# Performance work log

Hardware: AMD Instinct MI355X
Metric: run time of the kernel (lower is better)

The kernel has to match this reference:

```python
import jax, jax.numpy as jnp
import numpy as np


def setup_inputs() -> dict:
    key = jax.random.key(0)
    ks = jax.random.split(key, 6)
    B, H, N, C, O, G = 4, 24, 512, 120, 512, 5
    x = jax.random.normal(ks[0], (B, H, N, C), dtype=jnp.float32)
    t_indices = jnp.arange(H, dtype=jnp.int64)
    time_emb = jax.random.normal(ks[1], (H, 8), dtype=jnp.float32)
    # kaiming-uniform-ish init for base linear weight
    fan_in = C + 8
    bound = float(np.sqrt(6.0 / fan_in))
    base_w = jax.random.uniform(ks[2], (O, C + 8), minval=-bound, maxval=bound, dtype=jnp.float32)
    base_b = jax.random.uniform(ks[3], (O,), minval=-1.0 / np.sqrt(fan_in), maxval=1.0 / np.sqrt(fan_in), dtype=jnp.float32)
    spline_weight = jax.random.uniform(ks[4], (O, C + 8, G), minval=-0.1, maxval=0.1, dtype=jnp.float32)
    return {"x": x, "t_indices": t_indices, "time_emb": time_emb,
            "base_w": base_w, "base_b": base_b, "spline_weight": spline_weight}


def reference(x, t_indices, time_emb, base_w, base_b, spline_weight):
    B, H, N, C = x.shape
    G = spline_weight.shape[-1]
    grid = jnp.linspace(-1.0, 1.0, G, dtype=x.dtype)  # non-trainable buffer
    # time embedding lookup, broadcast over batch and nodes: [B,H,N,8]
    t_emb = jnp.broadcast_to(time_emb[t_indices][None, :, None, :], (B, H, N, time_emb.shape[-1]))
    x_in = jnp.concatenate([x, t_emb], axis=-1)  # [B,H,N,C+8]
    # base path: SiLU then linear
    base = jnp.einsum('bhni,oi->bhno', jax.nn.silu(x_in), base_w) + base_b
    # RBF basis: [B,H,N,C+8,G]
    inv_h = (G - 1) / 2.0  # 1 / (2/(G-1))
    basis = jnp.exp(-(((x_in[..., None] - grid) * inv_h) ** 2))
    spline = jnp.einsum('bhnig,oig->bhno', basis, spline_weight)
    return base + spline
```

## Files before the change

### kernel.cpp

```cpp
#include <hip/hip_runtime.h>
#include <hip/hip_bf16.h>

typedef __attribute__((ext_vector_type(4))) float f32x4;
typedef __attribute__((ext_vector_type(8))) short bf16x8;

#define GLDS16(gp, lp) __builtin_amdgcn_global_load_lds( \
    (__attribute__((address_space(1))) void*)(void*)(gp), \
    (__attribute__((address_space(3))) void*)(lp), 16, 0, 0)

static constexpr int Mtot = 49152;
static constexpr int Otot = 512;
static constexpr int Hh   = 24;

__device__ inline unsigned short f2bf(float f) {
    __hip_bfloat16 h = __float2bfloat16(f);
    unsigned short u;
    __builtin_memcpy(&u, &h, 2);
    return u;
}

static constexpr float C1 = 0.36787944117f;
static constexpr float C4 = 0.01831563889f;

__global__ __launch_bounds__(256) void prep_W(
        const float* __restrict__ bw, const float* __restrict__ sw,
        uint4* __restrict__ Wt)
{
    const int tid = blockIdx.x * 256 + threadIdx.x;
    const int col = tid & 511;
    const int cc  = tid >> 9;
    const int k0  = cc * 8;
    const float scale[6] = {1.0f, C4, C1, 1.0f, C1, C4};
    unsigned short s[8];
    #pragma unroll
    for (int e = 0; e < 8; ++e) {
        const int k = k0 + e;
        const int i = k / 6, f = k - i * 6;
        const float v = (f == 0) ? bw[col * 128 + i]
                                 : sw[(col * 128 + i) * 5 + (f - 1)] * scale[f];
        s[e] = f2bf(v);
    }
    uint4 u;
    u.x = s[0] | ((unsigned)s[1] << 16);
    u.y = s[2] | ((unsigned)s[3] << 16);
    u.z = s[4] | ((unsigned)s[5] << 16);
    u.w = s[6] | ((unsigned)s[7] << 16);
    Wt[tid] = u;
}

__global__ __launch_bounds__(256, 2) void gemm_kan(
        const float* __restrict__ x, const int* __restrict__ t_idx,
        const float* __restrict__ temb,
        const char* __restrict__ Wt,
        const float* __restrict__ bias,
        float* __restrict__ out)
{
    __shared__ char Alds[12 * 128 * 16];
    __shared__ char Blds[2][12 * 128 * 16];
    const int t    = threadIdx.x;
    const int wave = t >> 6;
    const int lane = t & 63;
    const int ll   = lane & 15;
    const int q4   = lane >> 4;
    const int wm   = (wave >> 1) * 64;
    const int wn   = (wave & 1) * 64;

    const int bid = blockIdx.x;
    const int swz = (bid & 7) * 192 + (bid >> 3);
    const int m_base = (swz >> 2) * 128;
    const int n_base = (swz & 3) * 128;

    const int row = t >> 1;
    const int hh  = t & 1;
    const int ht  = t_idx[(m_base >> 9) % Hh];
    const float* xrow = x + (size_t)(m_base + row) * 120;
    const float* trow = temb + ht * 8;

    auto chanptr = [&](int i0) -> const float* {
        return (i0 < 120) ? (xrow + i0) : (trow + (i0 - 120));
    };

    auto stageB = [&](int it, int buf) {
        #pragma unroll
        for (int j = 0; j < 6; ++j) {
            const int c = wave * 3 + (j >> 1);
            const int g = (j & 1) * 64;
            const char* src = Wt + (((size_t)(it * 12 + c) * 512 + n_base + g
                                     + lane) << 4);
            GLDS16(src, Blds[buf] + ((c * 128 + g) << 4));
        }
    };

    auto gen = [&](const float4 ca, const float4 cb, uint4* au) {
        const float v[8] = {ca.x, ca.y, ca.z, ca.w, cb.x, cb.y, cb.z, cb.w};
        unsigned short s[48];
        #pragma unroll
        for (int c = 0; c < 8; ++c) {
            const float vv = v[c];
            s[c * 6 + 0] = f2bf(vv * __builtin_amdgcn_rcpf(1.0f + __expf(-vv)));
            const float tt = __expf(-4.0f * vv * vv);
            const float uu = __expf(4.0f * vv);
            const float rr = __builtin_amdgcn_rcpf(uu);
            const float tu = tt * uu, tr = tt * rr;
            s[c * 6 + 1] = f2bf(tr * rr);
            s[c * 6 + 2] = f2bf(tr);
            s[c * 6 + 3] = f2bf(tt);
            s[c * 6 + 4] = f2bf(tu);
            s[c * 6 + 5] = f2bf(tu * uu);
        }
        #pragma unroll
        for (int j = 0; j < 6; ++j) {
            unsigned u[4];
            #pragma unroll
            for (int n = 0; n < 4; ++n)
                u[n] = s[j * 8 + 2 * n] | ((unsigned)s[j * 8 + 2 * n + 1] << 16);
            au[j] = make_uint4(u[0], u[1], u[2], u[3]);
        }
    };

    auto writeA = [&](const uint4* au) {
        #pragma unroll
        for (int j = 0; j < 6; ++j) {
            const int ck = 6 * hh + j;
            *(uint4*)(Alds + ((ck * 128 + row) << 4)) = au[j];
        }
    };

    f32x4 acc[4][4] = {};

    stageB(0, 0);
    float4 pa, pb;
    {
        const float* p0 = chanptr(hh * 8);
        const float4 xa = *(const float4*)p0;
        const float4 xb = *(const float4*)(p0 + 4);
        const float* p1 = chanptr(16 + hh * 8);
        pa = *(const float4*)p1;
        pb = *(const float4*)(p1 + 4);
        uint4 a0[6];
        gen(xa, xb, a0);
        writeA(a0);
    }
    __syncthreads();

    #pragma unroll
    for (int it = 0; it < 8; ++it) {
        if (it < 7) stageB(it + 1, (it + 1) & 1);

        const float4 ca = pa, cb = pb;
        if (it < 6) {
            const float* p = chanptr((it + 2) * 16 + hh * 8);
            pa = *(const float4*)p;
            pb = *(const float4*)(p + 4);
        }
        uint4 au[6];
        if (it < 7) gen(ca, cb, au);

        const char* B = Blds[it & 1];
        #pragma unroll
        for (int kk = 0; kk < 3; ++kk) {
            const int ch = kk * 4 + q4;
            bf16x8 af[4], bf[4];
            #pragma unroll
            for (int mi = 0; mi < 4; ++mi)
                af[mi] = *(const bf16x8*)(Alds + ((ch * 128 + wm + mi * 16 + ll) << 4));
            #pragma unroll
            for (int ni = 0; ni < 4; ++ni)
                bf[ni] = *(const bf16x8*)(B + ((ch * 128 + wn + ni * 16 + ll) << 4));
            #pragma unroll
            for (int mi = 0; mi < 4; ++mi)
                #pragma unroll
                for (int ni = 0; ni < 4; ++ni)
                    acc[mi][ni] = __builtin_amdgcn_mfma_f32_16x16x32_bf16(
                        af[mi], bf[ni], acc[mi][ni], 0, 0, 0);
        }

        if (it < 7) {
            __syncthreads();
            writeA(au);
            __syncthreads();
        }
    }

    const int col0 = n_base + wn + ll;
    const int row0 = m_base + wm + q4 * 4;
    #pragma unroll
    for (int ni = 0; ni < 4; ++ni) {
        const int col = col0 + ni * 16;
        const float bv = bias[col];
        #pragma unroll
        for (int mi = 0; mi < 4; ++mi) {
            #pragma unroll
            for (int r = 0; r < 4; ++r) {
                out[(long)(row0 + mi * 16 + r) * Otot + col] = acc[mi][ni][r] + bv;
            }
        }
    }
}

extern "C" void kernel_launch(void* const* d_in, const int* in_sizes, int n_in,
                              void* d_out, int out_size, void* d_ws, size_t ws_size,
                              hipStream_t stream) {
    const float* x    = (const float*)d_in[0];
    const int*   tidx = (const int*)  d_in[1];
    const float* temb = (const float*)d_in[2];
    const float* bw   = (const float*)d_in[3];
    const float* bb   = (const float*)d_in[4];
    const float* sw   = (const float*)d_in[5];
    float* out = (float*)d_out;

    char* Wt = (char*)d_ws;

    prep_W<<<49152 / 256, 256, 0, stream>>>(bw, sw, (uint4*)Wt);
    gemm_kan<<<1536, 256, 0, stream>>>(x, tidx, temb, Wt, bb, out);
}
```

Measured before the change: 172.4 us.

## Single-buffer B tile and interleave basis generation with MFMA for occupancy

Drops the B double buffer in LDS, cutting shared memory per block from 72 KB to 48 KB, and raises launch bounds to three blocks per CU. Basis generation is split per channel and interleaved between the MFMA k-steps, which lowers live register pressure. The B load for the next iteration is now issued only after a barrier at the end of the current compute, so global-to-LDS loads no longer overlap the MFMAs within a block. The design relies on the extra resident blocks to hide that latency instead.

```diff
diff --git a/kernel.cpp b/kernel.cpp
--- a/kernel.cpp
+++ b/kernel.cpp
@@ -48,7 +48,7 @@
     Wt[tid] = u;
 }
 
-__global__ __launch_bounds__(256, 2) void gemm_kan(
+__global__ __launch_bounds__(256, 3) void gemm_kan(
         const float* __restrict__ x, const int* __restrict__ t_idx,
         const float* __restrict__ temb,
         const char* __restrict__ Wt,
@@ -56,7 +56,7 @@
         float* __restrict__ out)
 {
     __shared__ char Alds[12 * 128 * 16];
-    __shared__ char Blds[2][12 * 128 * 16];
+    __shared__ char Blds[12 * 128 * 16];
     const int t    = threadIdx.x;
     const int wave = t >> 6;
     const int lane = t & 63;
@@ -80,83 +80,73 @@
         return (i0 < 120) ? (xrow + i0) : (trow + (i0 - 120));
     };
 
-    auto stageB = [&](int it, int buf) {
+    auto stageB = [&](int it) {
         #pragma unroll
         for (int j = 0; j < 6; ++j) {
             const int c = wave * 3 + (j >> 1);
             const int g = (j & 1) * 64;
             const char* src = Wt + (((size_t)(it * 12 + c) * 512 + n_base + g
                                      + lane) << 4);
-            GLDS16(src, Blds[buf] + ((c * 128 + g) << 4));
-        }
-    };
-
-    auto gen = [&](const float4 ca, const float4 cb, uint4* au) {
-        const float v[8] = {ca.x, ca.y, ca.z, ca.w, cb.x, cb.y, cb.z, cb.w};
-        unsigned short s[48];
-        #pragma unroll
-        for (int c = 0; c < 8; ++c) {
-            const float vv = v[c];
-            s[c * 6 + 0] = f2bf(vv * __builtin_amdgcn_rcpf(1.0f + __expf(-vv)));
-            const float tt = __expf(-4.0f * vv * vv);
-            const float uu = __expf(4.0f * vv);
-            const float rr = __builtin_amdgcn_rcpf(uu);
-            const float tu = tt * uu, tr = tt * rr;
-            s[c * 6 + 1] = f2bf(tr * rr);
-            s[c * 6 + 2] = f2bf(tr);
-            s[c * 6 + 3] = f2bf(tt);
-            s[c * 6 + 4] = f2bf(tu);
-            s[c * 6 + 5] = f2bf(tu * uu);
-        }
+            GLDS16(src, Blds + ((c * 128 + g) << 4));
+        }
+    };
+
+    auto genCh = [&](unsigned short* s, int c, float vv) {
+        s[c * 6 + 0] = f2bf(vv * __builtin_amdgcn_rcpf(1.0f + __expf(-vv)));
+        const float tt = __expf(-4.0f * vv * vv);
+        const float uu = __expf(4.0f * vv);
+        const float rr = __builtin_amdgcn_rcpf(uu);
+        const float tu = tt * uu, tr = tt * rr;
+        s[c * 6 + 1] = f2bf(tr * rr);
+        s[c * 6 + 2] = f2bf(tr);
+        s[c * 6 + 3] = f2bf(tt);
+        s[c * 6 + 4] = f2bf(tu);
+        s[c * 6 + 5] = f2bf(tu * uu);
+    };
+
+    auto packWriteA = [&](const unsigned short* s) {
         #pragma unroll
         for (int j = 0; j < 6; ++j) {
             unsigned u[4];
             #pragma unroll
             for (int n = 0; n < 4; ++n)
                 u[n] = s[j * 8 + 2 * n] | ((unsigned)s[j * 8 + 2 * n + 1] << 16);
-            au[j] = make_uint4(u[0], u[1], u[2], u[3]);
-        }
-    };
-
-    auto writeA = [&](const uint4* au) {
-        #pragma unroll
-        for (int j = 0; j < 6; ++j) {
-            const int ck = 6 * hh + j;
-            *(uint4*)(Alds + ((ck * 128 + row) << 4)) = au[j];
+            *(uint4*)(Alds + (((6 * hh + j) * 128 + row) << 4)) =
+                make_uint4(u[0], u[1], u[2], u[3]);
         }
     };
 
     f32x4 acc[4][4] = {};
-
-    stageB(0, 0);
-    float4 pa, pb;
+    unsigned short s[48];
+
+    stageB(0);
     {
         const float* p0 = chanptr(hh * 8);
-        const float4 xa = *(const float4*)p0;
-        const float4 xb = *(const float4*)(p0 + 4);
+        const float4 ga = *(const float4*)p0;
+        const float4 gb = *(const float4*)(p0 + 4);
+        const float gv[8] = {ga.x, ga.y, ga.z, ga.w, gb.x, gb.y, gb.z, gb.w};
+        #pragma unroll
+        for (int c = 0; c < 8; ++c) genCh(s, c, gv[c]);
+        packWriteA(s);
+    }
+    float4 xa, xb;
+    {
         const float* p1 = chanptr(16 + hh * 8);
-        pa = *(const float4*)p1;
-        pb = *(const float4*)(p1 + 4);
-        uint4 a0[6];
-        gen(xa, xb, a0);
-        writeA(a0);
+        xa = *(const float4*)p1;
+        xb = *(const float4*)(p1 + 4);
     }
     __syncthreads();
 
     #pragma unroll
     for (int it = 0; it < 8; ++it) {
-        if (it < 7) stageB(it + 1, (it + 1) & 1);
-
-        const float4 ca = pa, cb = pb;
+        const float4 ca = xa, cb = xb;
         if (it < 6) {
             const float* p = chanptr((it + 2) * 16 + hh * 8);
-            pa = *(const float4*)p;
-            pb = *(const float4*)(p + 4);
-        }
-        uint4 au[6];
-        if (it < 7) gen(ca, cb, au);
-
-        const char* B = Blds[it & 1];
+            xa = *(const float4*)p;
+            xb = *(const float4*)(p + 4);
+        }
+        const float gv[8] = {ca.x, ca.y, ca.z, ca.w, cb.x, cb.y, cb.z, cb.w};
+
         #pragma unroll
         for (int kk = 0; kk < 3; ++kk) {
             const int ch = kk * 4 + q4;
@@ -166,18 +156,25 @@
                 af[mi] = *(const bf16x8*)(Alds + ((ch * 128 + wm + mi * 16 + ll) << 4));
             #pragma unroll
             for (int ni = 0; ni < 4; ++ni)
-                bf[ni] = *(const bf16x8*)(B + ((ch * 128 + wn + ni * 16 + ll) << 4));
+                bf[ni] = *(const bf16x8*)(Blds + ((ch * 128 + wn + ni * 16 + ll) << 4));
             #pragma unroll
             for (int mi = 0; mi < 4; ++mi)
                 #pragma unroll
                 for (int ni = 0; ni < 4; ++ni)
                     acc[mi][ni] = __builtin_amdgcn_mfma_f32_16x16x32_bf16(
                         af[mi], bf[ni], acc[mi][ni], 0, 0, 0);
-        }
+            if (it < 7) {
+                const int c0 = kk * 3;
+                const int c1 = (kk == 2) ? 8 : c0 + 3;
+                #pragma unroll
+                for (int c = c0; c < c1; ++c) genCh(s, c, gv[c]);
+            }
+        }
+        __syncthreads();
 
         if (it < 7) {
-            __syncthreads();
-            writeA(au);
+            stageB(it + 1);
+            packWriteA(s);
             __syncthreads();
         }
     }
```

After: 164.3 us. 4.7% less time.
